# Kernel tuning notes

Measured on AMD Instinct MI355X. Metric: run time of the kernel, lower is better.

Reference implementation:

```python
import jax, jax.numpy as jnp
import numpy as np

NUM_HEADS = 32
NUM_GROUP_HEADS = 8
DIM_MODEL = 2048
DIM_K = 64
DIM_V = 64


def setup_inputs() -> dict:
    key = jax.random.key(0)
    ks = jax.random.split(key, 11)
    B, S = 1, 2048
    scale = 0.02
    inp = {
        "queries": jax.random.normal(ks[0], (B, S, DIM_MODEL), jnp.float32),
        "keys": jax.random.normal(ks[1], (B, S, DIM_MODEL), jnp.float32),
        "values": jax.random.normal(ks[2], (B, S, DIM_MODEL), jnp.float32),
        "Wq": jax.random.normal(ks[3], (DIM_MODEL, DIM_K * NUM_HEADS), jnp.float32) * scale,
        "bq": jnp.zeros((DIM_K * NUM_HEADS,), jnp.float32),
        "Wk": jax.random.normal(ks[4], (DIM_MODEL, DIM_K * NUM_GROUP_HEADS), jnp.float32) * scale,
        "bk": jnp.zeros((DIM_K * NUM_GROUP_HEADS,), jnp.float32),
        "Wv": jax.random.normal(ks[5], (DIM_MODEL, DIM_V * NUM_GROUP_HEADS), jnp.float32) * scale,
        "bv": jnp.zeros((DIM_V * NUM_GROUP_HEADS,), jnp.float32),
        "Wo": jax.random.normal(ks[6], (DIM_V * NUM_HEADS, DIM_MODEL), jnp.float32) * scale,
        "bo": jnp.zeros((DIM_MODEL,), jnp.float32),
    }
    return inp


def reference(queries, keys, values, Wq, bq, Wk, bk, Wv, bv, Wo, bo):
    B, Sq, _ = queries.shape
    _, Sk, _ = keys.shape
    H, G = NUM_HEADS, NUM_GROUP_HEADS
    repeats = H // G

    # projections -> [B, heads, S, d]
    q = (queries @ Wq + bq).reshape(B, Sq, H, DIM_K).transpose(0, 2, 1, 3)
    k = (keys @ Wk + bk).reshape(B, Sk, G, DIM_K).transpose(0, 2, 1, 3)
    v = (values @ Wv + bv).reshape(B, Sk, G, DIM_V).transpose(0, 2, 1, 3)

    # GQA: repeat each group head `repeats` times (repeat_interleave on head dim)
    k = jnp.repeat(k, repeats, axis=1)  # [B, H, Sk, dk]
    v = jnp.repeat(v, repeats, axis=1)  # [B, H, Sk, dv]

    scores = jnp.einsum("bhqd,bhkd->bhqk", q, k) / (DIM_K ** 0.5)
    causal = jnp.triu(jnp.ones((Sq, Sk), dtype=bool), k=1)
    scores = jnp.where(causal, -jnp.inf, scores)
    attn = jax.nn.softmax(scores, axis=-1)
    out = jnp.einsum("bhqk,bhkd->bhqd", attn, v)  # [B, H, Sq, dv]
    out = out.transpose(0, 2, 1, 3).reshape(B, Sq, H * DIM_V)
    return out @ Wo + bo
```

## Files before the change

### kernel.cpp

```cpp
#include <hip/hip_runtime.h>
#include <hip/hip_bf16.h>

#define S_LEN  2048
#define DMODEL 2048
#define NH     32
#define NG     8
#define DK     64
#define DV     64

typedef short bf16x8 __attribute__((ext_vector_type(8)));
typedef float f32x4  __attribute__((ext_vector_type(4)));

__device__ __forceinline__ ushort f32_to_bf16(float f) {
    uint u = __float_as_uint(f);
    return (ushort)((u + 0x7fffu + ((u >> 16) & 1u)) >> 16);
}
__device__ __forceinline__ float bf16_to_f32(ushort h) {
    return __uint_as_float(((uint)h) << 16);
}

__global__ void cast_f32_to_bf16(const float* __restrict__ in,
                                 ushort* __restrict__ out, int n8) {
    int i = blockIdx.x * blockDim.x + threadIdx.x;
    const int stride = gridDim.x * blockDim.x;
    for (; i < n8; i += stride) {
        const float4 a = ((const float4*)in)[2 * i];
        const float4 b = ((const float4*)in)[2 * i + 1];
        uint4 o;
        o.x = (uint)f32_to_bf16(a.x) | ((uint)f32_to_bf16(a.y) << 16);
        o.y = (uint)f32_to_bf16(a.z) | ((uint)f32_to_bf16(a.w) << 16);
        o.z = (uint)f32_to_bf16(b.x) | ((uint)f32_to_bf16(b.y) << 16);
        o.w = (uint)f32_to_bf16(b.z) | ((uint)f32_to_bf16(b.w) << 16);
        ((uint4*)out)[i] = o;
    }
}

__global__ void transpose_cast_bf16(const float* __restrict__ W,
                                    ushort* __restrict__ Wt, int K, int N) {
    __shared__ float t[32][33];
    const int n0 = blockIdx.x * 32, k0 = blockIdx.y * 32;
    const int tx = threadIdx.x, ty = threadIdx.y;
#pragma unroll
    for (int i = 0; i < 4; ++i)
        t[ty + 8 * i][tx] = W[(size_t)(k0 + ty + 8 * i) * N + n0 + tx];
    __syncthreads();
#pragma unroll
    for (int i = 0; i < 4; ++i)
        Wt[(size_t)(n0 + ty + 8 * i) * K + k0 + tx] = f32_to_bf16(t[tx][ty + 8 * i]);
}

__global__ void transpose_bf16(const ushort* __restrict__ in,
                               ushort* __restrict__ out, int R, int C) {
    __shared__ ushort t[32][34];
    const int c0 = blockIdx.x * 32, r0 = blockIdx.y * 32;
    const int tx = threadIdx.x, ty = threadIdx.y;
#pragma unroll
    for (int i = 0; i < 4; ++i)
        t[ty + 8 * i][tx] = in[(size_t)(r0 + ty + 8 * i) * C + c0 + tx];
    __syncthreads();
#pragma unroll
    for (int i = 0; i < 4; ++i)
        out[(size_t)(c0 + ty + 8 * i) * R + r0 + tx] = t[tx][ty + 8 * i];
}

template <bool OUT_F32>
__device__ __forceinline__ void gemm_body_128x64(
        const ushort* __restrict__ A, const ushort* __restrict__ Bt,
        const float* __restrict__ bias, void* __restrict__ Cv,
        ushort* As, ushort* Bs, int N, int K) {
    const int tid  = threadIdx.x;
    const int lane = tid & 63, wave = tid >> 6;
    const int l15 = lane & 15, quad = lane >> 4;
    const int row0 = blockIdx.y * 128, col0 = blockIdx.x * 64;

    f32x4 acc[2][4];
#pragma unroll
    for (int i = 0; i < 2; ++i)
#pragma unroll
        for (int j = 0; j < 4; ++j) { f32x4 z = {0.f,0.f,0.f,0.f}; acc[i][j] = z; }

    const int ar = tid >> 1, ak = (tid & 1) * 16;
    const int br = tid >> 2, bk = (tid & 3) * 8;
    const ushort* aptr = A  + (size_t)(row0 + ar) * K + ak;
    const ushort* bptr = Bt + (size_t)(col0 + br) * K + bk;

    bf16x8 a0 = *(const bf16x8*)(aptr);
    bf16x8 a1 = *(const bf16x8*)(aptr + 8);
    bf16x8 b0 = *(const bf16x8*)(bptr);

    for (int k0 = 0; k0 < K; k0 += 32) {
        __syncthreads();
        *(bf16x8*)&As[ar * 40 + ak]     = a0;
        *(bf16x8*)&As[ar * 40 + ak + 8] = a1;
        *(bf16x8*)&Bs[br * 40 + bk]     = b0;
        __syncthreads();

        if (k0 + 32 < K) {
            a0 = *(const bf16x8*)(aptr + k0 + 32);
            a1 = *(const bf16x8*)(aptr + k0 + 40);
            b0 = *(const bf16x8*)(bptr + k0 + 32);
        }

        bf16x8 af[2], bf[4];
#pragma unroll
        for (int mi = 0; mi < 2; ++mi)
            af[mi] = *(const bf16x8*)&As[(wave * 32 + mi * 16 + l15) * 40 + quad * 8];
#pragma unroll
        for (int ni = 0; ni < 4; ++ni)
            bf[ni] = *(const bf16x8*)&Bs[(ni * 16 + l15) * 40 + quad * 8];
#pragma unroll
        for (int mi = 0; mi < 2; ++mi)
#pragma unroll
            for (int ni = 0; ni < 4; ++ni)
                acc[mi][ni] = __builtin_amdgcn_mfma_f32_16x16x32_bf16(
                    af[mi], bf[ni], acc[mi][ni], 0, 0, 0);
    }

#pragma unroll
    for (int mi = 0; mi < 2; ++mi)
#pragma unroll
        for (int ni = 0; ni < 4; ++ni) {
            const int col = col0 + ni * 16 + l15;
            const float bv = bias[col];
#pragma unroll
            for (int reg = 0; reg < 4; ++reg) {
                const int row = row0 + wave * 32 + mi * 16 + quad * 4 + reg;
                const float val = acc[mi][ni][reg] + bv;
                if (OUT_F32)
                    ((float*)Cv)[(size_t)row * N + col] = val;
                else
                    ((ushort*)Cv)[(size_t)row * N + col] = f32_to_bf16(val);
            }
        }
}

template <bool OUT_F32>
__global__ __launch_bounds__(256) void gemm_bf16_v2(
        const ushort* __restrict__ A, const ushort* __restrict__ Bt,
        const float* __restrict__ bias, void* __restrict__ Cv, int N, int K) {
    __shared__ ushort As[128 * 40];
    __shared__ ushort Bs[64 * 40];
    gemm_body_128x64<OUT_F32>(A, Bt, bias, Cv, As, Bs, N, K);
}

__global__ __launch_bounds__(256) void gemm_kv(
        const ushort* __restrict__ Xk, const ushort* __restrict__ Xv,
        const ushort* __restrict__ Wkt, const ushort* __restrict__ Wvt,
        const float* __restrict__ bk, const float* __restrict__ bv,
        ushort* __restrict__ Kb, ushort* __restrict__ Vb, int N, int K) {
    __shared__ ushort As[128 * 40];
    __shared__ ushort Bs[64 * 40];
    if (blockIdx.z == 0)
        gemm_body_128x64<false>(Xk, Wkt, bk, Kb, As, Bs, N, K);
    else
        gemm_body_128x64<false>(Xv, Wvt, bv, Vb, As, Bs, N, K);
}

__global__ __launch_bounds__(256) void gqa_attn_mfma(
        const ushort* __restrict__ Qb, const ushort* __restrict__ Kb,
        const ushort* __restrict__ Vt, ushort* __restrict__ Ab) {
    __shared__ ushort Ks[64 * 72];
    __shared__ ushort Vs[64 * 72];
    __shared__ ushort Ps[4][16 * 72];

    const int h    = blockIdx.y, g = h >> 2;
    const int tid  = threadIdx.x;
    const int lane = tid & 63, wave = tid >> 6;
    const int l15  = lane & 15, quad = lane >> 4;
    const int NT   = S_LEN / 64;

    const int srow = tid >> 2, sch = tid & 3;
    const ushort* kbase = Kb + (size_t)srow * (NG * DK) + g * DK + sch * 16;
    const ushort* vbase = Vt + (size_t)(g * 64 + srow) * S_LEN + sch * 16;

    for (int sel = 0; sel < 2; ++sel) {
        const int qt = sel ? (NT - 1 - (int)blockIdx.x) : (int)blockIdx.x;
        const int qr = qt * 64 + wave * 16;

        bf16x8 qa0, qa1;
        {
            const size_t base = (size_t)(qr + l15) * (NH * DK) + (size_t)h * DK + quad * 8;
            qa0 = *(const bf16x8*)&Qb[base];
            qa1 = *(const bf16x8*)&Qb[base + 32];
        }

        f32x4 o[4];
#pragma unroll
        for (int dt = 0; dt < 4; ++dt) { f32x4 z = {0.f,0.f,0.f,0.f}; o[dt] = z; }
        float mrow[4] = {-1e30f, -1e30f, -1e30f, -1e30f};
        float lrow[4] = {0.f, 0.f, 0.f, 0.f};

        bf16x8 kr0 = *(const bf16x8*)(kbase);
        bf16x8 kr1 = *(const bf16x8*)(kbase + 8);
        bf16x8 vr0 = *(const bf16x8*)(vbase);
        bf16x8 vr1 = *(const bf16x8*)(vbase + 8);

        for (int jt = 0; jt <= qt; ++jt) {
            __syncthreads();
            *(bf16x8*)&Ks[srow * 72 + sch * 16]     = kr0;
            *(bf16x8*)&Ks[srow * 72 + sch * 16 + 8] = kr1;
            *(bf16x8*)&Vs[srow * 72 + sch * 16]     = vr0;
            *(bf16x8*)&Vs[srow * 72 + sch * 16 + 8] = vr1;
            __syncthreads();

            if (jt < qt) {
                const size_t ko = (size_t)(jt + 1) * 64 * (NG * DK);
                const size_t vo = (size_t)(jt + 1) * 64;
                kr0 = *(const bf16x8*)(kbase + ko);
                kr1 = *(const bf16x8*)(kbase + ko + 8);
                vr0 = *(const bf16x8*)(vbase + vo);
                vr1 = *(const bf16x8*)(vbase + vo + 8);
            }

            f32x4 s[4];
#pragma unroll
            for (int kt = 0; kt < 4; ++kt) {
                const bf16x8 kb0 = *(const bf16x8*)&Ks[(kt * 16 + l15) * 72 + quad * 8];
                const bf16x8 kb1 = *(const bf16x8*)&Ks[(kt * 16 + l15) * 72 + 32 + quad * 8];
                f32x4 acc = {0.f, 0.f, 0.f, 0.f};
                acc = __builtin_amdgcn_mfma_f32_16x16x32_bf16(qa0, kb0, acc, 0, 0, 0);
                acc = __builtin_amdgcn_mfma_f32_16x16x32_bf16(qa1, kb1, acc, 0, 0, 0);
                s[kt] = acc;
            }

            if (jt == qt) {
#pragma unroll
                for (int kt = 0; kt < 4; ++kt)
#pragma unroll
                    for (int r = 0; r < 4; ++r) {
                        const int key = kt * 16 + l15;
                        const int row = wave * 16 + quad * 4 + r;
                        s[kt][r] = (key <= row) ? s[kt][r] * 0.125f : -1e30f;
                    }
            } else {
#pragma unroll
                for (int kt = 0; kt < 4; ++kt)
#pragma unroll
                    for (int r = 0; r < 4; ++r) s[kt][r] *= 0.125f;
            }

            float rmax[4];
#pragma unroll
            for (int r = 0; r < 4; ++r)
                rmax[r] = fmaxf(fmaxf(s[0][r], s[1][r]), fmaxf(s[2][r], s[3][r]));
#pragma unroll
            for (int off = 1; off <= 8; off <<= 1)
#pragma unroll
                for (int r = 0; r < 4; ++r)
                    rmax[r] = fmaxf(rmax[r], __shfl_xor(rmax[r], off, 64));

            float alpha[4];
#pragma unroll
            for (int r = 0; r < 4; ++r) {
                const float mn = fmaxf(mrow[r], rmax[r]);
                alpha[r] = __expf(mrow[r] - mn);
                mrow[r] = mn;
            }

            float p[4][4], rsum[4];
#pragma unroll
            for (int kt = 0; kt < 4; ++kt)
#pragma unroll
                for (int r = 0; r < 4; ++r)
                    p[kt][r] = __expf(s[kt][r] - mrow[r]);
#pragma unroll
            for (int r = 0; r < 4; ++r)
                rsum[r] = (p[0][r] + p[1][r]) + (p[2][r] + p[3][r]);
#pragma unroll
            for (int off = 1; off <= 8; off <<= 1)
#pragma unroll
                for (int r = 0; r < 4; ++r)
                    rsum[r] += __shfl_xor(rsum[r], off, 64);
#pragma unroll
            for (int r = 0; r < 4; ++r)
                lrow[r] = lrow[r] * alpha[r] + rsum[r];
#pragma unroll
            for (int dt = 0; dt < 4; ++dt)
#pragma unroll
                for (int r = 0; r < 4; ++r)
                    o[dt][r] *= alpha[r];

            ushort* Pw = &Ps[wave][0];
#pragma unroll
            for (int kt = 0; kt < 4; ++kt)
#pragma unroll
                for (int r = 0; r < 4; ++r)
                    Pw[(quad * 4 + r) * 72 + kt * 16 + l15] = f32_to_bf16(p[kt][r]);
            const bf16x8 pa0 = *(const bf16x8*)&Pw[l15 * 72 + quad * 8];
            const bf16x8 pa1 = *(const bf16x8*)&Pw[l15 * 72 + 32 + quad * 8];

#pragma unroll
            for (int dt = 0; dt < 4; ++dt) {
                const bf16x8 vb0 = *(const bf16x8*)&Vs[(dt * 16 + l15) * 72 + quad * 8];
                const bf16x8 vb1 = *(const bf16x8*)&Vs[(dt * 16 + l15) * 72 + 32 + quad * 8];
                o[dt] = __builtin_amdgcn_mfma_f32_16x16x32_bf16(pa0, vb0, o[dt], 0, 0, 0);
                o[dt] = __builtin_amdgcn_mfma_f32_16x16x32_bf16(pa1, vb1, o[dt], 0, 0, 0);
            }
        }

        float inv[4];
#pragma unroll
        for (int r = 0; r < 4; ++r) inv[r] = 1.0f / lrow[r];
#pragma unroll
        for (int dt = 0; dt < 4; ++dt)
#pragma unroll
            for (int r = 0; r < 4; ++r)
                Ab[(size_t)(qr + quad * 4 + r) * (NH * DV) + (size_t)h * DV + dt * 16 + l15] =
                    f32_to_bf16(o[dt][r] * inv[r]);
    }
}

extern "C" void kernel_launch(void* const* d_in, const int* in_sizes, int n_in,
                              void* d_out, int out_size, void* d_ws, size_t ws_size,
                              hipStream_t stream) {
    const float* queries = (const float*)d_in[0];
    const float* keys    = (const float*)d_in[1];
    const float* values  = (const float*)d_in[2];
    const float* Wq      = (const float*)d_in[3];
    const float* bq      = (const float*)d_in[4];
    const float* Wk      = (const float*)d_in[5];
    const float* bk      = (const float*)d_in[6];
    const float* Wv      = (const float*)d_in[7];
    const float* bv      = (const float*)d_in[8];
    const float* Wo      = (const float*)d_in[9];
    const float* bo      = (const float*)d_in[10];
    float* out = (float*)d_out;

    const size_t MB = 1024 * 1024;
    unsigned char* w = (unsigned char*)d_ws;
    ushort* Xq  = (ushort*)(w + 0 * MB);
    ushort* Xk  = (ushort*)(w + 8 * MB);
    ushort* Xv  = (ushort*)(w + 16 * MB);
    ushort* Wqt = (ushort*)(w + 24 * MB);
    ushort* Wkt = (ushort*)(w + 32 * MB);
    ushort* Wvt = (ushort*)(w + 34 * MB);
    ushort* Wot = (ushort*)(w + 36 * MB);
    ushort* Qb  = (ushort*)(w + 44 * MB);
    ushort* Kb  = (ushort*)(w + 52 * MB);
    ushort* Vb  = (ushort*)(w + 54 * MB);
    ushort* Ab  = (ushort*)(w + 56 * MB);
    ushort* Vtp = (ushort*)(w + 8 * MB);

    const int n8 = (S_LEN * DMODEL) / 8;
    cast_f32_to_bf16<<<1024, 256, 0, stream>>>(queries, Xq, n8);
    cast_f32_to_bf16<<<1024, 256, 0, stream>>>(keys,    Xk, n8);
    cast_f32_to_bf16<<<1024, 256, 0, stream>>>(values,  Xv, n8);

    dim3 tb(32, 8);
    transpose_cast_bf16<<<dim3(2048 / 32, 2048 / 32), tb, 0, stream>>>(Wq, Wqt, DMODEL, 2048);
    transpose_cast_bf16<<<dim3(512 / 32,  2048 / 32), tb, 0, stream>>>(Wk, Wkt, DMODEL, 512);
    transpose_cast_bf16<<<dim3(512 / 32,  2048 / 32), tb, 0, stream>>>(Wv, Wvt, DMODEL, 512);
    transpose_cast_bf16<<<dim3(2048 / 32, 2048 / 32), tb, 0, stream>>>(Wo, Wot, DMODEL, 2048);

    gemm_bf16_v2<false><<<dim3(2048 / 64, 2048 / 128), 256, 0, stream>>>(
        Xq, Wqt, bq, Qb, 2048, DMODEL);
    gemm_kv<<<dim3(512 / 64, 2048 / 128, 2), 256, 0, stream>>>(
        Xk, Xv, Wkt, Wvt, bk, bv, Kb, Vb, 512, DMODEL);

    transpose_bf16<<<dim3(512 / 32, 2048 / 32), tb, 0, stream>>>(Vb, Vtp, S_LEN, 512);

    gqa_attn_mfma<<<dim3(16, 32), 256, 0, stream>>>(Qb, Kb, Vtp, Ab);

    gemm_bf16_v2<true><<<dim3(2048 / 64, 2048 / 128), 256, 0, stream>>>(
        Ab, Wot, bo, out, 2048, DMODEL);
}
```

Before: 326.0 us.

## Transpose score MFMA, fold softmax scale into Q, defer rescaling in attention

```diff
diff --git a/kernel.cpp b/kernel.cpp
--- a/kernel.cpp
+++ b/kernel.cpp
@@ -17,6 +17,9 @@
 }
 __device__ __forceinline__ float bf16_to_f32(ushort h) {
     return __uint_as_float(((uint)h) << 16);
+}
+__device__ __forceinline__ uint pack_bf16x2(float a, float b) {
+    return (uint)f32_to_bf16(a) | ((uint)f32_to_bf16(b) << 16);
 }
 
 __global__ void cast_f32_to_bf16(const float* __restrict__ in,
@@ -67,7 +70,7 @@
 __device__ __forceinline__ void gemm_body_128x64(
         const ushort* __restrict__ A, const ushort* __restrict__ Bt,
         const float* __restrict__ bias, void* __restrict__ Cv,
-        ushort* As, ushort* Bs, int N, int K) {
+        ushort* As, ushort* Bs, int N, int K, float scale) {
     const int tid  = threadIdx.x;
     const int lane = tid & 63, wave = tid >> 6;
     const int l15 = lane & 15, quad = lane >> 4;
@@ -125,7 +128,7 @@
 #pragma unroll
             for (int reg = 0; reg < 4; ++reg) {
                 const int row = row0 + wave * 32 + mi * 16 + quad * 4 + reg;
-                const float val = acc[mi][ni][reg] + bv;
+                const float val = (acc[mi][ni][reg] + bv) * scale;
                 if (OUT_F32)
                     ((float*)Cv)[(size_t)row * N + col] = val;
                 else
@@ -137,10 +140,11 @@
 template <bool OUT_F32>
 __global__ __launch_bounds__(256) void gemm_bf16_v2(
         const ushort* __restrict__ A, const ushort* __restrict__ Bt,
-        const float* __restrict__ bias, void* __restrict__ Cv, int N, int K) {
+        const float* __restrict__ bias, void* __restrict__ Cv, int N, int K,
+        float scale) {
     __shared__ ushort As[128 * 40];
     __shared__ ushort Bs[64 * 40];
-    gemm_body_128x64<OUT_F32>(A, Bt, bias, Cv, As, Bs, N, K);
+    gemm_body_128x64<OUT_F32>(A, Bt, bias, Cv, As, Bs, N, K, scale);
 }
 
 __global__ __launch_bounds__(256) void gemm_kv(
@@ -151,9 +155,9 @@
     __shared__ ushort As[128 * 40];
     __shared__ ushort Bs[64 * 40];
     if (blockIdx.z == 0)
-        gemm_body_128x64<false>(Xk, Wkt, bk, Kb, As, Bs, N, K);
+        gemm_body_128x64<false>(Xk, Wkt, bk, Kb, As, Bs, N, K, 1.0f);
     else
-        gemm_body_128x64<false>(Xv, Wvt, bv, Vb, As, Bs, N, K);
+        gemm_body_128x64<false>(Xv, Wvt, bv, Vb, As, Bs, N, K, 1.0f);
 }
 
 __global__ __launch_bounds__(256) void gqa_attn_mfma(
@@ -168,6 +172,7 @@
     const int lane = tid & 63, wave = tid >> 6;
     const int l15  = lane & 15, quad = lane >> 4;
     const int NT   = S_LEN / 64;
+    const float DEFER_THR = 11.5416f;
 
     const int srow = tid >> 2, sch = tid & 3;
     const ushort* kbase = Kb + (size_t)srow * (NG * DK) + g * DK + sch * 16;
@@ -187,8 +192,8 @@
         f32x4 o[4];
 #pragma unroll
         for (int dt = 0; dt < 4; ++dt) { f32x4 z = {0.f,0.f,0.f,0.f}; o[dt] = z; }
-        float mrow[4] = {-1e30f, -1e30f, -1e30f, -1e30f};
-        float lrow[4] = {0.f, 0.f, 0.f, 0.f};
+        float m = -1e30f;
+        float l = 0.f;
 
         bf16x8 kr0 = *(const bf16x8*)(kbase);
         bf16x8 kr1 = *(const bf16x8*)(kbase + 8);
@@ -218,74 +223,71 @@
                 const bf16x8 kb0 = *(const bf16x8*)&Ks[(kt * 16 + l15) * 72 + quad * 8];
                 const bf16x8 kb1 = *(const bf16x8*)&Ks[(kt * 16 + l15) * 72 + 32 + quad * 8];
                 f32x4 acc = {0.f, 0.f, 0.f, 0.f};
-                acc = __builtin_amdgcn_mfma_f32_16x16x32_bf16(qa0, kb0, acc, 0, 0, 0);
-                acc = __builtin_amdgcn_mfma_f32_16x16x32_bf16(qa1, kb1, acc, 0, 0, 0);
+                acc = __builtin_amdgcn_mfma_f32_16x16x32_bf16(kb0, qa0, acc, 0, 0, 0);
+                acc = __builtin_amdgcn_mfma_f32_16x16x32_bf16(kb1, qa1, acc, 0, 0, 0);
                 s[kt] = acc;
             }
 
             if (jt == qt) {
+                const int row = wave * 16 + l15;
 #pragma unroll
                 for (int kt = 0; kt < 4; ++kt)
 #pragma unroll
                     for (int r = 0; r < 4; ++r) {
-                        const int key = kt * 16 + l15;
-                        const int row = wave * 16 + quad * 4 + r;
-                        s[kt][r] = (key <= row) ? s[kt][r] * 0.125f : -1e30f;
+                        const int key = kt * 16 + quad * 4 + r;
+                        if (key > row) s[kt][r] = -1e30f;
                     }
-            } else {
-#pragma unroll
-                for (int kt = 0; kt < 4; ++kt)
-#pragma unroll
-                    for (int r = 0; r < 4; ++r) s[kt][r] *= 0.125f;
-            }
-
-            float rmax[4];
-#pragma unroll
-            for (int r = 0; r < 4; ++r)
-                rmax[r] = fmaxf(fmaxf(s[0][r], s[1][r]), fmaxf(s[2][r], s[3][r]));
-#pragma unroll
-            for (int off = 1; off <= 8; off <<= 1)
+            }
+
+            float pmax;
+            {
+                const float t0 = fmaxf(fmaxf(s[0][0], s[0][1]), fmaxf(s[0][2], s[0][3]));
+                const float t1 = fmaxf(fmaxf(s[1][0], s[1][1]), fmaxf(s[1][2], s[1][3]));
+                const float t2 = fmaxf(fmaxf(s[2][0], s[2][1]), fmaxf(s[2][2], s[2][3]));
+                const float t3 = fmaxf(fmaxf(s[3][0], s[3][1]), fmaxf(s[3][2], s[3][3]));
+                pmax = fmaxf(fmaxf(t0, t1), fmaxf(t2, t3));
+            }
+            pmax = fmaxf(pmax, __shfl_xor(pmax, 16, 64));
+            pmax = fmaxf(pmax, __shfl_xor(pmax, 32, 64));
+
+            if (!__all(pmax - m <= DEFER_THR)) {
+                const float mnew  = fmaxf(m, pmax);
+                const float alpha = __builtin_amdgcn_exp2f(m - mnew);
+                l *= alpha;
+#pragma unroll
+                for (int dt = 0; dt < 4; ++dt)
+#pragma unroll
+                    for (int r = 0; r < 4; ++r) o[dt][r] *= alpha;
+                m = mnew;
+            }
+
+            float p[4][4];
+#pragma unroll
+            for (int kt = 0; kt < 4; ++kt)
 #pragma unroll
                 for (int r = 0; r < 4; ++r)
-                    rmax[r] = fmaxf(rmax[r], __shfl_xor(rmax[r], off, 64));
-
-            float alpha[4];
-#pragma unroll
-            for (int r = 0; r < 4; ++r) {
-                const float mn = fmaxf(mrow[r], rmax[r]);
-                alpha[r] = __expf(mrow[r] - mn);
-                mrow[r] = mn;
-            }
-
-            float p[4][4], rsum[4];
-#pragma unroll
-            for (int kt = 0; kt < 4; ++kt)
-#pragma unroll
-                for (int r = 0; r < 4; ++r)
-                    p[kt][r] = __expf(s[kt][r] - mrow[r]);
-#pragma unroll
-            for (int r = 0; r < 4; ++r)
-                rsum[r] = (p[0][r] + p[1][r]) + (p[2][r] + p[3][r]);
-#pragma unroll
-            for (int off = 1; off <= 8; off <<= 1)
-#pragma unroll
-                for (int r = 0; r < 4; ++r)
-                    rsum[r] += __shfl_xor(rsum[r], off, 64);
-#pragma unroll
-            for (int r = 0; r < 4; ++r)
-                lrow[r] = lrow[r] * alpha[r] + rsum[r];
-#pragma unroll
-            for (int dt = 0; dt < 4; ++dt)
-#pragma unroll
-                for (int r = 0; r < 4; ++r)
-                    o[dt][r] *= alpha[r];
+                    p[kt][r] = __builtin_amdgcn_exp2f(s[kt][r] - m);
+
+            float rsum;
+            {
+                const float u0 = (p[0][0] + p[0][1]) + (p[0][2] + p[0][3]);
+                const float u1 = (p[1][0] + p[1][1]) + (p[1][2] + p[1][3]);
+                const float u2 = (p[2][0] + p[2][1]) + (p[2][2] + p[2][3]);
+                const float u3 = (p[3][0] + p[3][1]) + (p[3][2] + p[3][3]);
+                rsum = (u0 + u1) + (u2 + u3);
+            }
+            rsum += __shfl_xor(rsum, 16, 64);
+            rsum += __shfl_xor(rsum, 32, 64);
+            l += rsum;
 
             ushort* Pw = &Ps[wave][0];
 #pragma unroll
-            for (int kt = 0; kt < 4; ++kt)
-#pragma unroll
-                for (int r = 0; r < 4; ++r)
-                    Pw[(quad * 4 + r) * 72 + kt * 16 + l15] = f32_to_bf16(p[kt][r]);
+            for (int kt = 0; kt < 4; ++kt) {
+                uint2 uu;
+                uu.x = pack_bf16x2(p[kt][0], p[kt][1]);
+                uu.y = pack_bf16x2(p[kt][2], p[kt][3]);
+                *(uint2*)&Pw[l15 * 72 + kt * 16 + quad * 4] = uu;
+            }
             const bf16x8 pa0 = *(const bf16x8*)&Pw[l15 * 72 + quad * 8];
             const bf16x8 pa1 = *(const bf16x8*)&Pw[l15 * 72 + 32 + quad * 8];
 
@@ -293,20 +295,19 @@
             for (int dt = 0; dt < 4; ++dt) {
                 const bf16x8 vb0 = *(const bf16x8*)&Vs[(dt * 16 + l15) * 72 + quad * 8];
                 const bf16x8 vb1 = *(const bf16x8*)&Vs[(dt * 16 + l15) * 72 + 32 + quad * 8];
-                o[dt] = __builtin_amdgcn_mfma_f32_16x16x32_bf16(pa0, vb0, o[dt], 0, 0, 0);
-                o[dt] = __builtin_amdgcn_mfma_f32_16x16x32_bf16(pa1, vb1, o[dt], 0, 0, 0);
-            }
-        }
-
-        float inv[4];
-#pragma unroll
-        for (int r = 0; r < 4; ++r) inv[r] = 1.0f / lrow[r];
-#pragma unroll
-        for (int dt = 0; dt < 4; ++dt)
-#pragma unroll
-            for (int r = 0; r < 4; ++r)
-                Ab[(size_t)(qr + quad * 4 + r) * (NH * DV) + (size_t)h * DV + dt * 16 + l15] =
-                    f32_to_bf16(o[dt][r] * inv[r]);
+                o[dt] = __builtin_amdgcn_mfma_f32_16x16x32_bf16(vb0, pa0, o[dt], 0, 0, 0);
+                o[dt] = __builtin_amdgcn_mfma_f32_16x16x32_bf16(vb1, pa1, o[dt], 0, 0, 0);
+            }
+        }
+
+        const float invl = 1.0f / l;
+#pragma unroll
+        for (int dt = 0; dt < 4; ++dt) {
+            uint2 uu;
+            uu.x = pack_bf16x2(o[dt][0] * invl, o[dt][1] * invl);
+            uu.y = pack_bf16x2(o[dt][2] * invl, o[dt][3] * invl);
+            *(uint2*)&Ab[(size_t)(qr + l15) * (NH * DV) + (size_t)h * DV + dt * 16 + quad * 4] = uu;
+        }
     }
 }
 
@@ -352,8 +353,9 @@
     transpose_cast_bf16<<<dim3(512 / 32,  2048 / 32), tb, 0, stream>>>(Wv, Wvt, DMODEL, 512);
     transpose_cast_bf16<<<dim3(2048 / 32, 2048 / 32), tb, 0, stream>>>(Wo, Wot, DMODEL, 2048);
 
+    const float QSCALE = 0.125f * 1.44269504f;
     gemm_bf16_v2<false><<<dim3(2048 / 64, 2048 / 128), 256, 0, stream>>>(
-        Xq, Wqt, bq, Qb, 2048, DMODEL);
+        Xq, Wqt, bq, Qb, 2048, DMODEL, QSCALE);
     gemm_kv<<<dim3(512 / 64, 2048 / 128, 2), 256, 0, stream>>>(
         Xk, Xv, Wkt, Wvt, bk, bv, Kb, Vb, 512, DMODEL);
 
@@ -362,5 +364,5 @@
     gqa_attn_mfma<<<dim3(16, 32), 256, 0, stream>>>(Qb, Kb, Vtp, Ab);
 
     gemm_bf16_v2<true><<<dim3(2048 / 64, 2048 / 128), 256, 0, stream>>>(
-        Ab, Wot, bo, out, 2048, DMODEL);
-}
+        Ab, Wot, bo, out, 2048, DMODEL, 1.0f);
+}
```

Result: faster. 303.3 us (-7.0%).
